# Optimization experiments

Hardware: AMD Instinct MI355X
Metric: run time of the kernel (lower is better)

The kernel has to match this reference:

```python
import jax, jax.numpy as jnp
import numpy as np

N_NODES = 20000
N_EDGES = 40000
H = 64          # n_hidden
F_ATOM = 62     # n_atom_features (< H, triggers zero-pad path)
F_BOND = 6      # n_bond_features
B = 512         # number of graphs in batch
T = 2           # message passing steps


def setup_inputs() -> dict:
    key = jax.random.key(0)
    ks = jax.random.split(key, 20)
    s = 0.05  # small init scale to avoid selu/tanh saturation
    inp = {
        'node_features': jax.random.normal(ks[0], (N_NODES, F_ATOM), jnp.float32),
        'edge_features': jax.random.normal(ks[1], (N_EDGES, F_BOND), jnp.float32),
        'edge_domain': jax.random.randint(ks[2], (N_EDGES,), 0, N_NODES, jnp.int32),
        'edge_range': jax.random.randint(ks[3], (N_EDGES,), 0, N_NODES, jnp.int32),
        'graph_id': jnp.sort(jax.random.randint(ks[4], (N_NODES,), 0, B, jnp.int32)),
        # EdgeNetwork params (weights stored [in, out], i.e. torch W.T)
        'Wm': jax.random.normal(ks[5], (F_BOND, H), jnp.float32) * s,
        'bm': jnp.zeros((H,), jnp.float32),
        'Ew': jax.random.normal(ks[6], (H, H * H), jnp.float32) * s,  # E.weight used as mm(mlp, E.weight): [H, H*H]
        # update2 linears (T=2)
        'Wu0': jax.random.normal(ks[7], (H, H), jnp.float32) * s,
        'bu0': jnp.zeros((H,), jnp.float32),
        'Wu1': jax.random.normal(ks[8], (H, H), jnp.float32) * s,
        'bu1': jnp.zeros((H,), jnp.float32),
        # atom_embed
        'Wae': jax.random.normal(ks[9], (H, H), jnp.float32) * s,
        'bae': jnp.zeros((H,), jnp.float32),
        # AggregateReadout.R
        'WR': jax.random.normal(ks[10], (H, H), jnp.float32) * s,
        'bR': jnp.zeros((H,), jnp.float32),
        # mlp + out head
        'Wmlp': jax.random.normal(ks[11], (H, H), jnp.float32) * s,
        'bmlp': jnp.zeros((H,), jnp.float32),
        'Wout': jax.random.normal(ks[12], (H, 1), jnp.float32) * s,
        'bout': jnp.zeros((1,), jnp.float32),
    }
    return inp


def reference(node_features, edge_features, edge_domain, edge_range, graph_id,
              Wm, bm, Ew, Wu0, bu0, Wu1, bu1, Wae, bae, WR, bR,
              Wmlp, bmlp, Wout, bout):
    # pad node features up to n_hidden (original zero-pads when narrower)
    h = jnp.pad(node_features, ((0, 0), (0, H - F_ATOM)))  # [N, H]

    # EdgeNetwork: edge-conditioned per-edge HxH weight matrix.
    # Edge features are constant across T, so A is identical each step;
    # compute once (original recomputes the same values every iteration).
    mlp_features = jax.nn.relu(edge_features @ Wm + bm)      # [E, H]
    A = (mlp_features @ Ew).reshape(-1, H, H)                # [E, H, H]

    for Wu, bu in ((Wu0, bu0), (Wu1, bu1)):
        hj = h[edge_range]                                   # gather [E, H]
        edge_message = jnp.einsum('eij,ej->ei', A, hj)       # bmm [E, H]
        message = jax.ops.segment_sum(edge_message, edge_domain,
                                      num_segments=N_NODES)  # scatter-add [N, H]
        h = jax.nn.selu(message @ Wu + bu + h)

    atom_embedding = h @ Wae + bae                           # [N, H]
    # AggregateReadout
    atom_activation = jax.nn.selu(atom_embedding @ WR + bR)  # [N, H]
    graph_sum = jax.ops.segment_sum(atom_activation, graph_id, num_segments=B)
    graph_embedding = jnp.tanh(graph_sum)                    # [B, H]

    mlp_out = jax.nn.relu(graph_embedding @ Wmlp + bmlp)     # [B, H]
    out = mlp_out @ Wout + bout                              # [B, 1]
    return out.reshape(-1, 1)
```

## Files before the change

kernel.cpp:

```cpp
#include <hip/hip_runtime.h>
#include <math.h>

#define NN 20000
#define NE 40000
#define H 64
#define F_ATOM 62
#define F_BOND 6
#define NB 512

typedef _Float16 f16x8 __attribute__((ext_vector_type(8)));
typedef float f32x16 __attribute__((ext_vector_type(16)));

__device__ __forceinline__ float selu_f(float x) {
    const float scale = 1.0507009873554805f;
    const float alpha = 1.6732632423543772f;
    return scale * (x > 0.0f ? x : alpha * (__expf(x) - 1.0f));
}

__device__ __forceinline__ f16x8 splat8h(_Float16 x) {
    union { _Float16 h[2]; unsigned u; } p;
    p.h[0] = x; p.h[1] = x;
    union { unsigned u[4]; f16x8 v; } r;
    r.u[0] = p.u; r.u[1] = p.u; r.u[2] = p.u; r.u[3] = p.u;
    return r.v;
}

__global__ void prep_kernel(const float* __restrict__ nf, const float* __restrict__ ef,
                            const float* __restrict__ Wm, const float* __restrict__ bm,
                            const float* __restrict__ Ew,
                            float* __restrict__ h, _Float16* __restrict__ h_h,
                            unsigned* __restrict__ mlp2, _Float16* __restrict__ ewb,
                            float* __restrict__ msg, float* __restrict__ gsum) {
    const int bid = blockIdx.x;
    const int t = threadIdx.x;
    if (bid < 625) {
        __shared__ float st[64][65];
        const int el = t & 63;
        const int ig = t >> 6;
        const int e = bid * 64 + el;
        const float* efe = ef + e * F_BOND;
        const float e0 = efe[0], e1 = efe[1], e2 = efe[2];
        const float e3 = efe[3], e4 = efe[4], e5 = efe[5];
#pragma unroll
        for (int p = 0; p < 16; ++p) {
            const int i = ig * 16 + p;
            float s = bm[i];
            s = fmaf(e0, Wm[0 * H + i], s);
            s = fmaf(e1, Wm[1 * H + i], s);
            s = fmaf(e2, Wm[2 * H + i], s);
            s = fmaf(e3, Wm[3 * H + i], s);
            s = fmaf(e4, Wm[4 * H + i], s);
            s = fmaf(e5, Wm[5 * H + i], s);
            st[i][el] = fmaxf(s, 0.0f);
        }
        __syncthreads();
        const int p = t >> 3;
        const int ch = t & 7;
#pragma unroll
        for (int j = 0; j < 8; ++j) {
            const int e_l = ch * 8 + j;
            union { unsigned u; _Float16 hh[2]; } pk;
            pk.hh[0] = (_Float16)st[2 * p][e_l];
            pk.hh[1] = (_Float16)st[2 * p + 1][e_l];
            mlp2[(size_t)p * NE + bid * 64 + e_l] = pk.u;
        }
    } else if (bid < 5625) {
        int idx = (bid - 625) * 256 + t;
        int n = idx >> 6, c = idx & 63;
        float v = (c < F_ATOM) ? nf[n * F_ATOM + c] : 0.0f;
        h[idx] = v;
        h_h[idx] = (_Float16)v;
    } else if (bid < 5753) {
        int tid = (bid - 5625) * 256 + t;
        int l = tid & 63;
        int nt = (tid >> 6) & 1;
        int c = tid >> 7;
        int kk = c >> 2;
        int jbase = (c & 3) * 16 + (l >> 5) * 8;
        int i = nt * 32 + (l & 31);
        const float* src = Ew + kk * 4096 + i * 64 + jbase;
        _Float16* dst = ewb + tid * 8;
#pragma unroll
        for (int u = 0; u < 8; ++u) dst[u] = (_Float16)src[u];
    } else if (bid < 7003) {
        int idx = (bid - 5753) * 256 + t;
        reinterpret_cast<float4*>(msg)[idx] = make_float4(0.f, 0.f, 0.f, 0.f);
    } else {
        int idx = (bid - 7003) * 256 + t;
        reinterpret_cast<float4*>(gsum)[idx] = make_float4(0.f, 0.f, 0.f, 0.f);
    }
}

__global__ __launch_bounds__(256, 4) void edge_message_mfma(
    const _Float16* __restrict__ h_h, const unsigned* __restrict__ mlp2,
    const int* __restrict__ ed, const int* __restrict__ er,
    const _Float16* __restrict__ ewb, float* __restrict__ msg)
{
    __shared__ float4 smem4[2048];
    __shared__ int edom_s[64];

    const int t = threadIdx.x;
    const int w = t >> 6;
    const int lane = t & 63;
    const int l31 = lane & 31;
    const int hf = lane >> 5;
    const int mg = w & 1;
    const int kg = w >> 1;
    const int eb = blockIdx.x * 64;

    if (t < 64) edom_s[t] = ed[eb + t];

    const int e = eb + mg * 32 + l31;
    const int g0 = er[e];

    f16x8 hj[4];
#pragma unroll
    for (int cq = 0; cq < 4; ++cq)
        hj[cq] = *reinterpret_cast<const f16x8*>(h_h + g0 * 64 + cq * 16 + hf * 8);

    unsigned mv[16];
#pragma unroll
    for (int pp = 0; pp < 16; ++pp)
        mv[pp] = mlp2[(size_t)(kg * 16 + pp) * NE + e];

    char* sm = reinterpret_cast<char*>(smem4);
    auto stage = [&](int s) {
        const char* gs = reinterpret_cast<const char*>(ewb) +
                         ((size_t)(kg * 32 + s) << 13) + (mg << 12) + lane * 16;
        char* lb = sm + ((size_t)(kg * 2 + (s & 1)) << 13) + (mg << 12) + lane * 16;
#pragma unroll
        for (int r = 0; r < 4; ++r) {
            __builtin_amdgcn_global_load_lds(
                (const __attribute__((address_space(1))) void*)(gs + r * 1024),
                (__attribute__((address_space(3))) void*)(lb + r * 1024),
                16, 0, 0);
        }
    };

    f32x16 acc0, acc1;
#pragma unroll
    for (int i = 0; i < 16; ++i) { acc0[i] = 0.f; acc1[i] = 0.f; }

    stage(0);

#pragma unroll
    for (int s = 0; s < 32; ++s) {
        __syncthreads();
        if (s < 31) stage(s + 1);
        const char* buf = sm + ((size_t)(kg * 2 + (s & 1)) << 13);
        union { unsigned u; _Float16 hh[2]; } ua;
        ua.u = mv[s >> 1];
        f16x8 sA = splat8h(ua.hh[s & 1]);
#pragma unroll
        for (int cq = 0; cq < 4; ++cq) {
            f16x8 b0 = *reinterpret_cast<const f16x8*>(buf + (cq * 2 + 0) * 1024 + lane * 16);
            f16x8 b1 = *reinterpret_cast<const f16x8*>(buf + (cq * 2 + 1) * 1024 + lane * 16);
            f16x8 aA = sA * hj[cq];
            acc0 = __builtin_amdgcn_mfma_f32_32x32x16_f16(aA, b0, acc0, 0, 0, 0);
            acc1 = __builtin_amdgcn_mfma_f32_32x32x16_f16(aA, b1, acc1, 0, 0, 0);
        }
    }

    float* X = reinterpret_cast<float*>(smem4);
    __syncthreads();
    if (kg == 1) {
#pragma unroll
        for (int r = 0; r < 16; ++r) {
            const int m = (r & 3) + 8 * (r >> 2) + 4 * hf;
            X[(mg * 32 + m) * 64 + l31]      = acc0[r];
            X[(mg * 32 + m) * 64 + 32 + l31] = acc1[r];
        }
    }
    __syncthreads();
    if (kg == 0) {
#pragma unroll
        for (int r = 0; r < 16; ++r) {
            const int m = (r & 3) + 8 * (r >> 2) + 4 * hf;
            const int dom = edom_s[mg * 32 + m];
            atomicAdd(&msg[dom * 64 + l31],      acc0[r] + X[(mg * 32 + m) * 64 + l31]);
            atomicAdd(&msg[dom * 64 + 32 + l31], acc1[r] + X[(mg * 32 + m) * 64 + 32 + l31]);
        }
    }
}

__global__ void node_update_kernel(float* __restrict__ msg, const float* __restrict__ Wu,
                                   const float* __restrict__ bu, float* __restrict__ h,
                                   _Float16* __restrict__ h_h) {
    __shared__ float ms[4][68];
    int t = threadIdx.x;
    int nb = blockIdx.x * 4;
    int ln = t >> 6, i = t & 63;
    int o = (nb + ln) * H + i;
    ms[ln][i] = msg[o];
    msg[o] = 0.0f;
    __syncthreads();
    float s = bu[i];
#pragma unroll
    for (int k = 0; k < H; ++k) s = fmaf(ms[ln][k], Wu[k * H + i], s);
    float v = selu_f(s + h[o]);
    h[o] = v;
    h_h[o] = (_Float16)v;
}

__global__ void embed_readout_kernel(const float* __restrict__ h, const float* __restrict__ Wae,
                                     const float* __restrict__ bae, const float* __restrict__ WR,
                                     const float* __restrict__ bR, const int* __restrict__ gid,
                                     float* __restrict__ gsum) {
    __shared__ float hs[4][68];
    __shared__ float as_[4][68];
    int t = threadIdx.x;
    int nb = blockIdx.x * 4;
    int ln = t >> 6, i = t & 63;
    hs[ln][i] = h[(nb + ln) * H + i];
    __syncthreads();
    float s = bae[i];
#pragma unroll
    for (int k = 0; k < H; ++k) s = fmaf(hs[ln][k], Wae[k * H + i], s);
    as_[ln][i] = s;
    __syncthreads();
    float s2 = bR[i];
#pragma unroll
    for (int k = 0; k < H; ++k) s2 = fmaf(as_[ln][k], WR[k * H + i], s2);
    atomicAdd(&gsum[gid[nb + ln] * H + i], selu_f(s2));
}

__global__ void final_kernel(const float* __restrict__ gsum, const float* __restrict__ Wmlp,
                             const float* __restrict__ bmlp, const float* __restrict__ Wout,
                             const float* __restrict__ bout, float* __restrict__ out) {
    __shared__ float ge[64];
    int g = blockIdx.x, i = threadIdx.x;
    ge[i] = tanhf(gsum[g * H + i]);
    __syncthreads();
    float s = bmlp[i];
#pragma unroll
    for (int k = 0; k < H; ++k) s = fmaf(ge[k], Wmlp[k * H + i], s);
    float mo = fmaxf(s, 0.0f) * Wout[i];
#pragma unroll
    for (int off = 32; off > 0; off >>= 1) mo += __shfl_down(mo, off);
    if (i == 0) out[g] = mo + bout[0];
}

extern "C" void kernel_launch(void* const* d_in, const int* in_sizes, int n_in,
                              void* d_out, int out_size, void* d_ws, size_t ws_size,
                              hipStream_t stream) {
    const float* nf   = (const float*)d_in[0];
    const float* ef   = (const float*)d_in[1];
    const int*   ed   = (const int*)d_in[2];
    const int*   er   = (const int*)d_in[3];
    const int*   gid  = (const int*)d_in[4];
    const float* Wm   = (const float*)d_in[5];
    const float* bm   = (const float*)d_in[6];
    const float* Ew   = (const float*)d_in[7];
    const float* Wu0  = (const float*)d_in[8];
    const float* bu0  = (const float*)d_in[9];
    const float* Wu1  = (const float*)d_in[10];
    const float* bu1  = (const float*)d_in[11];
    const float* Wae  = (const float*)d_in[12];
    const float* bae  = (const float*)d_in[13];
    const float* WR   = (const float*)d_in[14];
    const float* bR   = (const float*)d_in[15];
    const float* Wmlp = (const float*)d_in[16];
    const float* bmlp = (const float*)d_in[17];
    const float* Wout = (const float*)d_in[18];
    const float* bout = (const float*)d_in[19];
    float* out = (float*)d_out;

    float* ws = (float*)d_ws;
    float*    h    = ws;
    float*    msg  = ws + 1280000;
    float*    gsum = ws + 2560000;
    unsigned* mlp2 = (unsigned*)(ws + 2592768);
    _Float16* h_h  = (_Float16*)(ws + 3872768);
    _Float16* ewb  = (_Float16*)(ws + 4512768);

    prep_kernel<<<7035, 256, 0, stream>>>(nf, ef, Wm, bm, Ew, h, h_h, mlp2, ewb, msg, gsum);

    for (int stepi = 0; stepi < 2; ++stepi) {
        edge_message_mfma<<<625, 256, 0, stream>>>(h_h, mlp2, ed, er, ewb, msg);
        node_update_kernel<<<NN / 4, 256, 0, stream>>>(msg, stepi ? Wu1 : Wu0,
                                                       stepi ? bu1 : bu0, h, h_h);
    }

    embed_readout_kernel<<<NN / 4, 256, 0, stream>>>(h, Wae, bae, WR, bR, gid, gsum);
    final_kernel<<<NB, 64, 0, stream>>>(gsum, Wmlp, bmlp, Wout, bout, out);
}
```

Measured before the change: 133.3 us.

## Have each wave process both edge halves to reuse staged Ew tiles

```diff
diff --git a/kernel.cpp b/kernel.cpp
--- a/kernel.cpp
+++ b/kernel.cpp
@@ -91,7 +91,7 @@
     }
 }
 
-__global__ __launch_bounds__(256, 4) void edge_message_mfma(
+__global__ __launch_bounds__(128, 2) void edge_message_mfma(
     const _Float16* __restrict__ h_h, const unsigned* __restrict__ mlp2,
     const int* __restrict__ ed, const int* __restrict__ er,
     const _Float16* __restrict__ ewb, float* __restrict__ msg)
@@ -100,36 +100,39 @@
     __shared__ int edom_s[64];
 
     const int t = threadIdx.x;
-    const int w = t >> 6;
     const int lane = t & 63;
+    const int kg = t >> 6;
     const int l31 = lane & 31;
     const int hf = lane >> 5;
-    const int mg = w & 1;
-    const int kg = w >> 1;
     const int eb = blockIdx.x * 64;
 
     if (t < 64) edom_s[t] = ed[eb + t];
 
-    const int e = eb + mg * 32 + l31;
-    const int g0 = er[e];
-
-    f16x8 hj[4];
-#pragma unroll
-    for (int cq = 0; cq < 4; ++cq)
-        hj[cq] = *reinterpret_cast<const f16x8*>(h_h + g0 * 64 + cq * 16 + hf * 8);
-
-    unsigned mv[16];
-#pragma unroll
-    for (int pp = 0; pp < 16; ++pp)
-        mv[pp] = mlp2[(size_t)(kg * 16 + pp) * NE + e];
+    const int eA = eb + l31;
+    const int eB = eA + 32;
+    const int gA = er[eA], gB = er[eB];
+
+    f16x8 hjA[4], hjB[4];
+#pragma unroll
+    for (int cq = 0; cq < 4; ++cq) {
+        hjA[cq] = *reinterpret_cast<const f16x8*>(h_h + gA * 64 + cq * 16 + hf * 8);
+        hjB[cq] = *reinterpret_cast<const f16x8*>(h_h + gB * 64 + cq * 16 + hf * 8);
+    }
+
+    unsigned mvA[16], mvB[16];
+#pragma unroll
+    for (int pp = 0; pp < 16; ++pp) {
+        mvA[pp] = mlp2[(size_t)(kg * 16 + pp) * NE + eA];
+        mvB[pp] = mlp2[(size_t)(kg * 16 + pp) * NE + eB];
+    }
 
     char* sm = reinterpret_cast<char*>(smem4);
     auto stage = [&](int s) {
         const char* gs = reinterpret_cast<const char*>(ewb) +
-                         ((size_t)(kg * 32 + s) << 13) + (mg << 12) + lane * 16;
-        char* lb = sm + ((size_t)(kg * 2 + (s & 1)) << 13) + (mg << 12) + lane * 16;
-#pragma unroll
-        for (int r = 0; r < 4; ++r) {
+                         ((size_t)(kg * 32 + s) << 13) + lane * 16;
+        char* lb = sm + ((size_t)(kg * 2 + (s & 1)) << 13) + lane * 16;
+#pragma unroll
+        for (int r = 0; r < 8; ++r) {
             __builtin_amdgcn_global_load_lds(
                 (const __attribute__((address_space(1))) void*)(gs + r * 1024),
                 (__attribute__((address_space(3))) void*)(lb + r * 1024),
@@ -137,9 +140,9 @@
         }
     };
 
-    f32x16 acc0, acc1;
-#pragma unroll
-    for (int i = 0; i < 16; ++i) { acc0[i] = 0.f; acc1[i] = 0.f; }
+    f32x16 a00, a01, a10, a11;
+#pragma unroll
+    for (int i = 0; i < 16; ++i) { a00[i] = 0.f; a01[i] = 0.f; a10[i] = 0.f; a11[i] = 0.f; }
 
     stage(0);
 
@@ -148,16 +151,20 @@
         __syncthreads();
         if (s < 31) stage(s + 1);
         const char* buf = sm + ((size_t)(kg * 2 + (s & 1)) << 13);
-        union { unsigned u; _Float16 hh[2]; } ua;
-        ua.u = mv[s >> 1];
+        union { unsigned u; _Float16 hh[2]; } ua, ub;
+        ua.u = mvA[s >> 1]; ub.u = mvB[s >> 1];
         f16x8 sA = splat8h(ua.hh[s & 1]);
+        f16x8 sB = splat8h(ub.hh[s & 1]);
 #pragma unroll
         for (int cq = 0; cq < 4; ++cq) {
             f16x8 b0 = *reinterpret_cast<const f16x8*>(buf + (cq * 2 + 0) * 1024 + lane * 16);
             f16x8 b1 = *reinterpret_cast<const f16x8*>(buf + (cq * 2 + 1) * 1024 + lane * 16);
-            f16x8 aA = sA * hj[cq];
-            acc0 = __builtin_amdgcn_mfma_f32_32x32x16_f16(aA, b0, acc0, 0, 0, 0);
-            acc1 = __builtin_amdgcn_mfma_f32_32x32x16_f16(aA, b1, acc1, 0, 0, 0);
+            f16x8 aA = sA * hjA[cq];
+            f16x8 aB = sB * hjB[cq];
+            a00 = __builtin_amdgcn_mfma_f32_32x32x16_f16(aA, b0, a00, 0, 0, 0);
+            a01 = __builtin_amdgcn_mfma_f32_32x32x16_f16(aA, b1, a01, 0, 0, 0);
+            a10 = __builtin_amdgcn_mfma_f32_32x32x16_f16(aB, b0, a10, 0, 0, 0);
+            a11 = __builtin_amdgcn_mfma_f32_32x32x16_f16(aB, b1, a11, 0, 0, 0);
         }
     }
 
@@ -167,8 +174,10 @@
 #pragma unroll
         for (int r = 0; r < 16; ++r) {
             const int m = (r & 3) + 8 * (r >> 2) + 4 * hf;
-            X[(mg * 32 + m) * 64 + l31]      = acc0[r];
-            X[(mg * 32 + m) * 64 + 32 + l31] = acc1[r];
+            X[m * 64 + l31]             = a00[r];
+            X[m * 64 + 32 + l31]        = a01[r];
+            X[(32 + m) * 64 + l31]      = a10[r];
+            X[(32 + m) * 64 + 32 + l31] = a11[r];
         }
     }
     __syncthreads();
@@ -176,9 +185,12 @@
 #pragma unroll
         for (int r = 0; r < 16; ++r) {
             const int m = (r & 3) + 8 * (r >> 2) + 4 * hf;
-            const int dom = edom_s[mg * 32 + m];
-            atomicAdd(&msg[dom * 64 + l31],      acc0[r] + X[(mg * 32 + m) * 64 + l31]);
-            atomicAdd(&msg[dom * 64 + 32 + l31], acc1[r] + X[(mg * 32 + m) * 64 + 32 + l31]);
+            const int domA = edom_s[m];
+            const int domB = edom_s[32 + m];
+            atomicAdd(&msg[domA * 64 + l31],      a00[r] + X[m * 64 + l31]);
+            atomicAdd(&msg[domA * 64 + 32 + l31], a01[r] + X[m * 64 + 32 + l31]);
+            atomicAdd(&msg[domB * 64 + l31],      a10[r] + X[(32 + m) * 64 + l31]);
+            atomicAdd(&msg[domB * 64 + 32 + l31], a11[r] + X[(32 + m) * 64 + 32 + l31]);
         }
     }
 }
@@ -276,7 +288,7 @@
     prep_kernel<<<7035, 256, 0, stream>>>(nf, ef, Wm, bm, Ew, h, h_h, mlp2, ewb, msg, gsum);
 
     for (int stepi = 0; stepi < 2; ++stepi) {
-        edge_message_mfma<<<625, 256, 0, stream>>>(h_h, mlp2, ed, er, ewb, msg);
+        edge_message_mfma<<<625, 128, 0, stream>>>(h_h, mlp2, ed, er, ewb, msg);
         node_update_kernel<<<NN / 4, 256, 0, stream>>>(msg, stepi ? Wu1 : Wu0,
                                                        stepi ? bu1 : bu0, h, h_h);
     }
```

Result: no change. 133.8 us (+0.4%).
